# Kernel optimization log

Hardware: AMD Instinct MI355X
Metric: run time of the kernel (lower is better)

Reference implementation:

```python
import jax, jax.numpy as jnp
import numpy as np

D_MODEL = 1024
N_HEADS = 16
D_K = D_MODEL // N_HEADS
ROPE_THETA = 10000.0


def setup_inputs() -> dict:
    key = jax.random.key(0)
    ks = jax.random.split(key, 5)
    B, S = 2, 2048
    std = (2.0 / (D_MODEL + D_MODEL)) ** 0.5
    x = jax.random.normal(ks[0], (B, S, D_MODEL), dtype=jnp.float32)
    Wq = jax.random.normal(ks[1], (D_MODEL, D_MODEL), dtype=jnp.float32) * std
    Wk = jax.random.normal(ks[2], (D_MODEL, D_MODEL), dtype=jnp.float32) * std
    Wv = jax.random.normal(ks[3], (D_MODEL, D_MODEL), dtype=jnp.float32) * std
    Wo = jax.random.normal(ks[4], (D_MODEL, D_MODEL), dtype=jnp.float32) * std
    token_positions = jnp.arange(S, dtype=jnp.int64 if jax.config.jax_enable_x64 else jnp.int32)
    return {"x": x, "Wq": Wq, "Wk": Wk, "Wv": Wv, "Wo": Wo,
            "token_positions": token_positions}


def _apply_rope(t, token_positions):
    # t: [B, H, S, d_k]; token_positions: [S]
    inv_freq = 1.0 / (ROPE_THETA ** (jnp.arange(0, D_K, 2, dtype=jnp.float32) / D_K))  # [d_k/2]
    freqs = token_positions.astype(jnp.float32)[:, None] * inv_freq[None, :]  # [S, d_k/2]
    cos, sin = jnp.cos(freqs), jnp.sin(freqs)
    x1, x2 = t[..., ::2], t[..., 1::2]
    xr = x1 * cos - x2 * sin
    yr = x1 * sin + x2 * cos
    # interleave back to even/odd positions
    out = jnp.stack([xr, yr], axis=-1).reshape(t.shape)
    return out


def reference(x, Wq, Wk, Wv, Wo, token_positions):
    B, S, D = x.shape
    H, dk = N_HEADS, D_K
    # projections: weight is [d_out, d_in], applied as x @ W.T
    def proj_heads(W):
        y = jnp.einsum('bsd,ed->bse', x, W)
        return y.reshape(B, S, H, dk).transpose(0, 2, 1, 3)  # [B,H,S,dk]
    q = proj_heads(Wq)
    k = proj_heads(Wk)
    v = proj_heads(Wv)
    q = _apply_rope(q, token_positions)
    k = _apply_rope(k, token_positions)
    scores = jnp.einsum('bhqd,bhkd->bhqk', q, k) / jnp.sqrt(jnp.float32(dk))
    causal = jnp.tril(jnp.ones((S, S), dtype=bool))
    scores = jnp.where(causal, scores, -jnp.inf)
    attn = jax.nn.softmax(scores, axis=-1)
    out = jnp.einsum('bhqk,bhkd->bhqd', attn, v)  # [B,H,S,dk]
    out = out.transpose(0, 2, 1, 3).reshape(B, S, D)
    return jnp.einsum('bsd,ed->bse', out, Wo)
```

## Files before the change

kernel.cpp:

```cpp
#include <hip/hip_runtime.h>

typedef __bf16 bf16x8 __attribute__((ext_vector_type(8)));
typedef float f32x4 __attribute__((ext_vector_type(4)));
typedef unsigned short u16x8 __attribute__((ext_vector_type(8)));


__device__ __forceinline__ unsigned short f2bf(float f) {
  unsigned u = __builtin_bit_cast(unsigned, f);
  u = (u + 0x7FFFu + ((u >> 16) & 1u)) >> 16;
  return (unsigned short)u;
}

__device__ __forceinline__ void load_lds16(const void* g, void* l) {
  __builtin_amdgcn_global_load_lds(
      (__attribute__((address_space(1))) void*)g,
      (__attribute__((address_space(3))) void*)l, 16, 0, 0);
}

__global__ __launch_bounds__(256) void k_convert(
    const float* __restrict__ x,
    const float* __restrict__ wq, const float* __restrict__ wk,
    const float* __restrict__ wv, const float* __restrict__ wo,
    unsigned short* __restrict__ xb,
    unsigned short* __restrict__ wqb, unsigned short* __restrict__ wkb,
    unsigned short* __restrict__ wvb, unsigned short* __restrict__ wob) {
  const int g = blockIdx.x * 256 + threadIdx.x;
  const float* src;
  unsigned short* dst;
  int off;
  if (g < (1 << 20)) {
    src = x; dst = xb; off = g;
  } else {
    const int q = g - (1 << 20);
    const int t = q >> 18;
    off = q & ((1 << 18) - 1);
    src = (t == 0) ? wq : (t == 1) ? wk : (t == 2) ? wv : wo;
    dst = (t == 0) ? wqb : (t == 1) ? wkb : (t == 2) ? wvb : wob;
  }
  const float4 v = ((const float4*)src)[off];
  ushort4 r;
  r.x = f2bf(v.x); r.y = f2bf(v.y); r.z = f2bf(v.z); r.w = f2bf(v.w);
  ((ushort4*)dst)[off] = r;
}

__global__ __launch_bounds__(256) void k_rope_tab(const int* __restrict__ tpos,
                                                  float* __restrict__ ct,
                                                  float* __restrict__ st) {
  const int idx = blockIdx.x * 256 + threadIdx.x;
  const int s = idx >> 5, i = idx & 31;
  const double p = (double)tpos[s];
  const double f = p * pow(10000.0, -(double)(2 * i) / 64.0);
  ct[idx] = (float)cos(f);
  st[idx] = (float)sin(f);
}

__device__ __forceinline__ void gemm_core_1024(
    const unsigned short* __restrict__ Ag,
    const unsigned short* __restrict__ Bg,
    unsigned short* As, unsigned short* Bs, f32x4 (&acc)[4][4], int tid) {
  const int lane = tid & 63;
  const int w = tid >> 6;
  const int wm = (w >> 1) * 64;
  const int wn = (w & 1) * 64;
  const int lr = lane & 15;
  const int lg8 = (lane >> 4) * 8;
  const int c0 = tid, c1 = 256 + tid;
  const int ar0 = c0 >> 2, ac0 = (c0 & 3) * 8;
  const int ar1 = c1 >> 2, ac1 = (c1 & 3) * 8;

  auto stage = [&](int buf, int kt) {
    unsigned short* Ab = As + buf * 4096;
    unsigned short* Bb = Bs + buf * 4096;
    load_lds16(Ag + ar0 * 1024 + kt + ac0, Ab + c0 * 8);
    load_lds16(Ag + ar1 * 1024 + kt + ac1, Ab + c1 * 8);
    load_lds16(Bg + ar0 * 1024 + kt + ac0, Bb + c0 * 8);
    load_lds16(Bg + ar1 * 1024 + kt + ac1, Bb + c1 * 8);
  };

  stage(0, 0);
  stage(1, 32);
  int cur = 0;
  for (int ki = 0; ki < 32; ++ki) {
    if (ki + 2 < 32) {
      int nb = cur + 2; if (nb >= 3) nb -= 3;
      stage(nb, (ki + 2) * 32);
      asm volatile("s_waitcnt vmcnt(8)" ::: "memory");
    } else if (ki + 1 < 32) {
      asm volatile("s_waitcnt vmcnt(4)" ::: "memory");
    } else {
      asm volatile("s_waitcnt vmcnt(0)" ::: "memory");
    }
    __builtin_amdgcn_s_barrier();
    const unsigned short* Ab = As + cur * 4096;
    const unsigned short* Bb = Bs + cur * 4096;
    bf16x8 af[4], bfv[4];
#pragma unroll
    for (int mi = 0; mi < 4; ++mi)
      af[mi] = *(const bf16x8*)(Ab + (wm + mi * 16 + lr) * 32 + lg8);
#pragma unroll
    for (int ni = 0; ni < 4; ++ni)
      bfv[ni] = *(const bf16x8*)(Bb + (wn + ni * 16 + lr) * 32 + lg8);
    __builtin_amdgcn_s_setprio(1);
#pragma unroll
    for (int mi = 0; mi < 4; ++mi)
#pragma unroll
      for (int ni = 0; ni < 4; ++ni)
        acc[mi][ni] = __builtin_amdgcn_mfma_f32_16x16x32_bf16(
            af[mi], bfv[ni], acc[mi][ni], 0, 0, 0);
    __builtin_amdgcn_s_setprio(0);
    __builtin_amdgcn_s_barrier();
    ++cur; if (cur == 3) cur = 0;
  }
}

__global__ __launch_bounds__(256) void k_proj(
    const unsigned short* __restrict__ Xb,
    const unsigned short* __restrict__ Wq, const unsigned short* __restrict__ Wk,
    const unsigned short* __restrict__ Wv,
    const float* __restrict__ ctab, const float* __restrict__ stab,
    unsigned short* __restrict__ Qo, unsigned short* __restrict__ Ko,
    unsigned short* __restrict__ Vo) {
  __shared__ __align__(16) unsigned short As[3 * 128 * 32];
  __shared__ __align__(16) unsigned short Bs[3 * 128 * 32];
  const int z = blockIdx.z;
  const unsigned short* Wsel = (z == 0) ? Wq : (z == 1) ? Wk : Wv;
  unsigned short* Out = (z == 0) ? Qo : (z == 1) ? Ko : Vo;
  const int tid = threadIdx.x;
  const int bm = blockIdx.x * 128, bn = blockIdx.y * 128;
  f32x4 acc[4][4] = {};
  gemm_core_1024(Xb + (size_t)bm * 1024, Wsel + (size_t)bn * 1024, As, Bs, acc, tid);

  const int lane = tid & 63, w = tid >> 6;
  const int wm = (w >> 1) * 64, wn = (w & 1) * 64;
  const int lr = lane & 15, lg = lane >> 4;
  const bool rope = (z < 2);
  const bool odd = lane & 1;
#pragma unroll
  for (int mi = 0; mi < 4; ++mi) {
#pragma unroll
    for (int ni = 0; ni < 4; ++ni) {
#pragma unroll
      for (int reg = 0; reg < 4; ++reg) {
        const int r = bm + wm + mi * 16 + lg * 4 + reg;
        const int e = bn + wn + ni * 16 + lr;
        float val = acc[mi][ni][reg];
        const float partner = __shfl_xor(val, 1);
        const int s = r & 2047, b = r >> 11;
        const int h = e >> 6, d = e & 63;
        float outv = val;
        if (rope) {
          const int i = d >> 1;
          const float c = ctab[s * 32 + i];
          const float sn = stab[s * 32 + i];
          outv = odd ? (val * c + partner * sn) : (val * c - partner * sn);
        }
        if (z == 2)
          Out[((size_t)(b * 16 + h) * 64 + d) * 2048 + s] = f2bf(outv);
        else
          Out[((size_t)(b * 16 + h) * 2048 + s) * 64 + d] = f2bf(outv);
      }
    }
  }
}

__global__ __launch_bounds__(256, 2) void k_attn(
    const unsigned short* __restrict__ Q, const unsigned short* __restrict__ K,
    const unsigned short* __restrict__ Vt, unsigned short* __restrict__ O) {
  __shared__ __align__(16) unsigned short Vs[4][64 * 64];
  __shared__ __align__(16) unsigned short Pl[4][32 * 68];
  const int L = blockIdx.x + 16 * blockIdx.y;
  const int rr = L & 31;
  const int bh = (rr & 7) * 4 + (rr >> 3);
  const int a = L >> 5;
  const int qt = (a < 8) ? a : 23 - a;
  const int tid = threadIdx.x, lane = tid & 63, w = tid >> 6;
  const int lr = lane & 15, lg = lane >> 4;
  const unsigned short* Qg = Q + (size_t)bh * 2048 * 64;
  const unsigned short* Kg = K + (size_t)bh * 2048 * 64;
  const unsigned short* Vg = Vt + (size_t)bh * 64 * 2048;
  const int qrow = qt * 128 + w * 32;
  const int Tw = (qrow + 95) >> 6;
  unsigned short* Vw = &Vs[w][0];
  unsigned short* Pw = &Pl[w][0];

  bf16x8 qf[2][2];
#pragma unroll
  for (int mi = 0; mi < 2; ++mi)
#pragma unroll
    for (int h = 0; h < 2; ++h)
      qf[mi][h] = *(const bf16x8*)(Qg + (qrow + mi * 16 + lr) * 64 + h * 32 + lg * 8);

  u16x8 ouv;
#pragma unroll
  for (int j = 0; j < 8; ++j) ouv[j] = 0x3F80;
  const bf16x8 onesf = __builtin_bit_cast(bf16x8, ouv);

  f32x4 oacc[2][4] = {};
  float mrow[2][4], lrow[2][4];
#pragma unroll
  for (int mi = 0; mi < 2; ++mi)
#pragma unroll
    for (int r = 0; r < 4; ++r) { mrow[mi][r] = -__builtin_inff(); lrow[mi][r] = 0.f; }

  const float SCL = 0.125f * 1.44269504088896f;

  auto issueV = [&](int kv0) {
#pragma unroll
    for (int i = 0; i < 8; ++i) {
      const int r = i * 8 + (lane >> 3);
      const int j = lane & 7;
      load_lds16(Vg + (size_t)r * 2048 + kv0 + ((j ^ (r & 7)) * 8),
                 Vw + i * 512 + lane * 8);
    }
  };
  auto loadK = [&](bf16x8 (&kd)[4][2], int kv0) {
#pragma unroll
    for (int nt = 0; nt < 4; ++nt)
#pragma unroll
      for (int h = 0; h < 2; ++h)
        kd[nt][h] = *(const bf16x8*)(Kg + (size_t)(kv0 + nt * 16 + lr) * 64 +
                                     h * 32 + lg * 8);
  };

  bf16x8 kA[4][2], kB[4][2];
  loadK(kA, 0);
  issueV(0);

  auto body = [&](int t, bf16x8 (&kc)[4][2], bf16x8 (&kn)[4][2]) {
    const int kv0 = t * 64;
    const bool more = (t + 1 < Tw);
    if (more) loadK(kn, kv0 + 64);

    f32x4 sacc[2][4];
    __builtin_amdgcn_s_setprio(1);
#pragma unroll
    for (int nt = 0; nt < 4; ++nt) {
#pragma unroll
      for (int mi = 0; mi < 2; ++mi) {
        f32x4 z = {0.f, 0.f, 0.f, 0.f};
        z = __builtin_amdgcn_mfma_f32_16x16x32_bf16(qf[mi][0], kc[nt][0], z, 0, 0, 0);
        sacc[mi][nt] = __builtin_amdgcn_mfma_f32_16x16x32_bf16(qf[mi][1], kc[nt][1], z, 0, 0, 0);
      }
    }
    __builtin_amdgcn_s_setprio(0);

    const bool needmask = (t == Tw - 1);
    float pm[2][4];
#pragma unroll
    for (int mi = 0; mi < 2; ++mi)
#pragma unroll
      for (int r = 0; r < 4; ++r) pm[mi][r] = -__builtin_inff();
#pragma unroll
    for (int mi = 0; mi < 2; ++mi)
#pragma unroll
      for (int nt = 0; nt < 4; ++nt)
#pragma unroll
        for (int reg = 0; reg < 4; ++reg) {
          float sv = sacc[mi][nt][reg];
          if (needmask) {
            const int kg = kv0 + nt * 16 + lr;
            const int qg = qrow + mi * 16 + lg * 4 + reg;
            if (kg > qg) sv = -__builtin_inff();
          }
          sacc[mi][nt][reg] = sv;
          pm[mi][reg] = fmaxf(pm[mi][reg], sv);
        }
#pragma unroll
    for (int off = 1; off < 16; off <<= 1)
#pragma unroll
      for (int mi = 0; mi < 2; ++mi)
#pragma unroll
        for (int reg = 0; reg < 4; ++reg)
          pm[mi][reg] = fmaxf(pm[mi][reg], __shfl_xor(pm[mi][reg], off));

    float gm = -1.f;
#pragma unroll
    for (int mi = 0; mi < 2; ++mi)
#pragma unroll
      for (int reg = 0; reg < 4; ++reg)
        gm = fmaxf(gm, pm[mi][reg] - mrow[mi][reg]);
    float al[2][4], msc[2][4];
    if (__any(gm > 0.f)) {
#pragma unroll
      for (int mi = 0; mi < 2; ++mi)
#pragma unroll
        for (int reg = 0; reg < 4; ++reg) {
          const float mn = fmaxf(mrow[mi][reg], pm[mi][reg]);
          al[mi][reg] = exp2f(SCL * (mrow[mi][reg] - mn));
          mrow[mi][reg] = mn;
          msc[mi][reg] = SCL * mn;
#pragma unroll
          for (int nt = 0; nt < 4; ++nt) oacc[mi][nt][reg] *= al[mi][reg];
          lrow[mi][reg] *= al[mi][reg];
        }
    } else {
#pragma unroll
      for (int mi = 0; mi < 2; ++mi)
#pragma unroll
        for (int reg = 0; reg < 4; ++reg) msc[mi][reg] = SCL * mrow[mi][reg];
    }
#pragma unroll
    for (int mi = 0; mi < 2; ++mi)
#pragma unroll
      for (int nt = 0; nt < 4; ++nt)
#pragma unroll
        for (int reg = 0; reg < 4; ++reg)
          sacc[mi][nt][reg] = exp2f(sacc[mi][nt][reg] * SCL - msc[mi][reg]);

#pragma unroll
    for (int mi = 0; mi < 2; ++mi)
#pragma unroll
      for (int nt = 0; nt < 4; ++nt)
#pragma unroll
        for (int reg = 0; reg < 4; ++reg)
          Pw[(mi * 16 + lg * 4 + reg) * 68 + nt * 16 + lr] =
              f2bf(sacc[mi][nt][reg]);
    bf16x8 pa[2][2];
#pragma unroll
    for (int mi = 0; mi < 2; ++mi)
#pragma unroll
      for (int ks = 0; ks < 2; ++ks)
        pa[mi][ks] = *(const bf16x8*)(Pw + (mi * 16 + lr) * 68 + ks * 32 + lg * 8);

    if (more) asm volatile("s_waitcnt vmcnt(8)" ::: "memory");
    else      asm volatile("s_waitcnt vmcnt(0)" ::: "memory");

    __builtin_amdgcn_s_setprio(1);
#pragma unroll
    for (int mi = 0; mi < 2; ++mi) {
      f32x4 z = {0.f, 0.f, 0.f, 0.f};
      z = __builtin_amdgcn_mfma_f32_16x16x32_bf16(pa[mi][0], onesf, z, 0, 0, 0);
      z = __builtin_amdgcn_mfma_f32_16x16x32_bf16(pa[mi][1], onesf, z, 0, 0, 0);
#pragma unroll
      for (int reg = 0; reg < 4; ++reg) lrow[mi][reg] += z[reg];
    }
#pragma unroll
    for (int nt = 0; nt < 4; ++nt) {
      const int row = nt * 16 + lr;
      const bf16x8 vb0 = *(const bf16x8*)(Vw + row * 64 + ((lg ^ (row & 7)) * 8));
      const bf16x8 vb1 = *(const bf16x8*)(Vw + row * 64 + (((lg + 4) ^ (row & 7)) * 8));
#pragma unroll
      for (int mi = 0; mi < 2; ++mi) {
        oacc[mi][nt] = __builtin_amdgcn_mfma_f32_16x16x32_bf16(pa[mi][0], vb0,
                                                               oacc[mi][nt], 0, 0, 0);
        oacc[mi][nt] = __builtin_amdgcn_mfma_f32_16x16x32_bf16(pa[mi][1], vb1,
                                                               oacc[mi][nt], 0, 0, 0);
      }
    }
    __builtin_amdgcn_s_setprio(0);

    asm volatile("s_waitcnt lgkmcnt(0)" ::: "memory");
    if (more) issueV(kv0 + 64);
  };

  int t = 0;
  while (t < Tw) {
    body(t, kA, kB); ++t;
    if (t < Tw) { body(t, kB, kA); ++t; }
  }

  const int b = bh >> 4, h = bh & 15;
#pragma unroll
  for (int mi = 0; mi < 2; ++mi)
#pragma unroll
    for (int reg = 0; reg < 4; ++reg) {
      const float inv = 1.0f / lrow[mi][reg];
      const int s = qrow + mi * 16 + lg * 4 + reg;
#pragma unroll
      for (int nt = 0; nt < 4; ++nt) {
        const int dv = nt * 16 + lr;
        O[((size_t)b * 2048 + s) * 1024 + h * 64 + dv] = f2bf(oacc[mi][nt][reg] * inv);
      }
    }
}

__global__ __launch_bounds__(256) void k_out(const unsigned short* __restrict__ Ab,
                                             const unsigned short* __restrict__ Wo,
                                             float* __restrict__ Out) {
  __shared__ __align__(16) unsigned short As[3 * 128 * 32];
  __shared__ __align__(16) unsigned short Bs[3 * 128 * 32];
  const int tid = threadIdx.x;
  const int bm = blockIdx.x * 128, bn = blockIdx.y * 128;
  f32x4 acc[4][4] = {};
  gemm_core_1024(Ab + (size_t)bm * 1024, Wo + (size_t)bn * 1024, As, Bs, acc, tid);
  const int lane = tid & 63, w = tid >> 6;
  const int wm = (w >> 1) * 64, wn = (w & 1) * 64;
  const int lr = lane & 15, lg = lane >> 4;
#pragma unroll
  for (int mi = 0; mi < 4; ++mi)
#pragma unroll
    for (int ni = 0; ni < 4; ++ni)
#pragma unroll
      for (int reg = 0; reg < 4; ++reg) {
        const int r = bm + wm + mi * 16 + lg * 4 + reg;
        const int e = bn + wn + ni * 16 + lr;
        Out[(size_t)r * 1024 + e] = acc[mi][ni][reg];
      }
}

extern "C" void kernel_launch(void* const* d_in, const int* in_sizes, int n_in,
                              void* d_out, int out_size, void* d_ws, size_t ws_size,
                              hipStream_t stream) {
  const float* x = (const float*)d_in[0];
  const float* Wq = (const float*)d_in[1];
  const float* Wk = (const float*)d_in[2];
  const float* Wv = (const float*)d_in[3];
  const float* Wo = (const float*)d_in[4];
  const int* tpos = (const int*)d_in[5];
  float* out = (float*)d_out;
  char* ws = (char*)d_ws;
  const size_t MB = 1024 * 1024;
  unsigned short* xb = (unsigned short*)(ws);
  unsigned short* wqb = (unsigned short*)(ws + 8 * MB);
  unsigned short* wkb = (unsigned short*)(ws + 10 * MB);
  unsigned short* wvb = (unsigned short*)(ws + 12 * MB);
  unsigned short* wob = (unsigned short*)(ws + 14 * MB);
  unsigned short* Qb = (unsigned short*)(ws + 16 * MB);
  unsigned short* Kb = (unsigned short*)(ws + 24 * MB);
  unsigned short* Vtb = (unsigned short*)(ws + 32 * MB);
  unsigned short* Ab = (unsigned short*)(ws + 40 * MB);
  float* ctab = (float*)(ws + 48 * MB);
  float* stab = (float*)(ws + 48 * MB + 256 * 1024);

  k_convert<<<dim3(8192), dim3(256), 0, stream>>>(x, Wq, Wk, Wv, Wo, xb, wqb, wkb,
                                                  wvb, wob);
  k_rope_tab<<<dim3(256), dim3(256), 0, stream>>>(tpos, ctab, stab);
  k_proj<<<dim3(32, 8, 3), dim3(256), 0, stream>>>(xb, wqb, wkb, wvb, ctab, stab,
                                                   Qb, Kb, Vtb);
  k_attn<<<dim3(16, 32), dim3(256), 0, stream>>>(Qb, Kb, Vtb, Ab);
  k_out<<<dim3(32, 8), dim3(256), 0, stream>>>(Ab, wob, out);
}
```

Measured before the change: 185.0 us.

## Split attention into single-wave blocks pairing a short and long causal query tile

The attention kernel now launches 2048 single-wavefront blocks instead of 512 four-wave blocks. Each wave handles two 16-row query tiles, one near the start and one near the end of the sequence, so causal work per wave is balanced and every block does similar work. The two tiles share the same K register loads and V tiles staged in LDS. This trades per-block LDS sharing and 32-row MFMA reuse for finer load balance, at the cost of more blocks and more per-iteration branching.

```diff
diff --git a/kernel.cpp b/kernel.cpp
--- a/kernel.cpp
+++ b/kernel.cpp
@@ -163,215 +163,215 @@
   }
 }
 
-__global__ __launch_bounds__(256, 2) void k_attn(
+__global__ __launch_bounds__(64, 2) void k_attn(
     const unsigned short* __restrict__ Q, const unsigned short* __restrict__ K,
     const unsigned short* __restrict__ Vt, unsigned short* __restrict__ O) {
-  __shared__ __align__(16) unsigned short Vs[4][64 * 64];
-  __shared__ __align__(16) unsigned short Pl[4][32 * 68];
-  const int L = blockIdx.x + 16 * blockIdx.y;
-  const int rr = L & 31;
-  const int bh = (rr & 7) * 4 + (rr >> 3);
-  const int a = L >> 5;
-  const int qt = (a < 8) ? a : 23 - a;
-  const int tid = threadIdx.x, lane = tid & 63, w = tid >> 6;
+  __shared__ __align__(16) unsigned short Vs[64 * 64];
+  __shared__ __align__(16) unsigned short Pl[32 * 68];
+  const int L = blockIdx.x;
+  const int bh = (L & 7) * 4 + ((L >> 3) & 3);
+  const int p = L >> 5;
+  const int qrowA = p * 16, qrowB = (127 - p) * 16;
+  const int lane = threadIdx.x & 63;
   const int lr = lane & 15, lg = lane >> 4;
   const unsigned short* Qg = Q + (size_t)bh * 2048 * 64;
   const unsigned short* Kg = K + (size_t)bh * 2048 * 64;
   const unsigned short* Vg = Vt + (size_t)bh * 64 * 2048;
-  const int qrow = qt * 128 + w * 32;
-  const int Tw = (qrow + 95) >> 6;
-  unsigned short* Vw = &Vs[w][0];
-  unsigned short* Pw = &Pl[w][0];
-
-  bf16x8 qf[2][2];
-#pragma unroll
-  for (int mi = 0; mi < 2; ++mi)
-#pragma unroll
-    for (int h = 0; h < 2; ++h)
-      qf[mi][h] = *(const bf16x8*)(Qg + (qrow + mi * 16 + lr) * 64 + h * 32 + lg * 8);
+  const int Ta = (qrowA + 79) >> 6;
+  const int Tb = (qrowB + 79) >> 6;
+
+  bf16x8 qfA[2], qfB[2];
+#pragma unroll
+  for (int h = 0; h < 2; ++h) {
+    qfA[h] = *(const bf16x8*)(Qg + (qrowA + lr) * 64 + h * 32 + lg * 8);
+    qfB[h] = *(const bf16x8*)(Qg + (qrowB + lr) * 64 + h * 32 + lg * 8);
+  }
 
   u16x8 ouv;
 #pragma unroll
   for (int j = 0; j < 8; ++j) ouv[j] = 0x3F80;
   const bf16x8 onesf = __builtin_bit_cast(bf16x8, ouv);
 
-  f32x4 oacc[2][4] = {};
-  float mrow[2][4], lrow[2][4];
-#pragma unroll
-  for (int mi = 0; mi < 2; ++mi)
-#pragma unroll
-    for (int r = 0; r < 4; ++r) { mrow[mi][r] = -__builtin_inff(); lrow[mi][r] = 0.f; }
+  f32x4 oA[4] = {}, oB[4] = {};
+  float mA[4], lA[4], mB[4], lB[4];
+#pragma unroll
+  for (int r = 0; r < 4; ++r) {
+    mA[r] = -__builtin_inff(); lA[r] = 0.f;
+    mB[r] = -__builtin_inff(); lB[r] = 0.f;
+  }
 
   const float SCL = 0.125f * 1.44269504088896f;
 
-  auto issueV = [&](int kv0) {
-#pragma unroll
-    for (int i = 0; i < 8; ++i) {
-      const int r = i * 8 + (lane >> 3);
-      const int j = lane & 7;
-      load_lds16(Vg + (size_t)r * 2048 + kv0 + ((j ^ (r & 7)) * 8),
-                 Vw + i * 512 + lane * 8);
-    }
+  const int kbase = lr * 64 + lg * 8;
+  const unsigned short* Knext = Kg;
+  const int vbase = (lane >> 3) * 2048 + (((lane & 7) ^ (lane >> 3)) * 8);
+  const unsigned short* Vnext = Vg;
+  unsigned short* Vw = &Vs[0];
+
+  auto loadK = [&](bf16x8 (&kd)[4][2]) {
+#pragma unroll
+    for (int nt = 0; nt < 4; ++nt)
+#pragma unroll
+      for (int h = 0; h < 2; ++h)
+        kd[nt][h] = *(const bf16x8*)(Knext + nt * 1024 + h * 32 + kbase);
+    Knext += 4096;
   };
-  auto loadK = [&](bf16x8 (&kd)[4][2], int kv0) {
+  auto issueV = [&]() {
+#pragma unroll
+    for (int i0 = 0; i0 < 8; ++i0)
+      load_lds16(Vnext + i0 * 16384 + vbase, Vw + i0 * 512 + lane * 8);
+    Vnext += 64;
+  };
+
+  auto softmax = [&](f32x4 (&s)[4], float (&m)[4], float (&l)[4], f32x4 (&oa)[4],
+                     int qrow, bool needmask, int kv0, int rowbase) {
+    float pm[4];
+#pragma unroll
+    for (int r = 0; r < 4; ++r) pm[r] = -__builtin_inff();
 #pragma unroll
     for (int nt = 0; nt < 4; ++nt)
 #pragma unroll
-      for (int h = 0; h < 2; ++h)
-        kd[nt][h] = *(const bf16x8*)(Kg + (size_t)(kv0 + nt * 16 + lr) * 64 +
-                                     h * 32 + lg * 8);
+      for (int reg = 0; reg < 4; ++reg) {
+        float sv = s[nt][reg];
+        if (needmask) {
+          const int kg = kv0 + nt * 16 + lr;
+          const int qg = qrow + lg * 4 + reg;
+          if (kg > qg) sv = -__builtin_inff();
+        }
+        s[nt][reg] = sv;
+        pm[reg] = fmaxf(pm[reg], sv);
+      }
+#pragma unroll
+    for (int off = 1; off < 16; off <<= 1)
+#pragma unroll
+      for (int reg = 0; reg < 4; ++reg)
+        pm[reg] = fmaxf(pm[reg], __shfl_xor(pm[reg], off));
+
+    float gm = -1.f;
+#pragma unroll
+    for (int reg = 0; reg < 4; ++reg) gm = fmaxf(gm, pm[reg] - m[reg]);
+    float msc[4];
+    if (__any(gm > 0.f)) {
+#pragma unroll
+      for (int reg = 0; reg < 4; ++reg) {
+        const float mn = fmaxf(m[reg], pm[reg]);
+        const float al = exp2f(SCL * (m[reg] - mn));
+        m[reg] = mn;
+        msc[reg] = SCL * mn;
+        l[reg] *= al;
+#pragma unroll
+        for (int nt = 0; nt < 4; ++nt) oa[nt][reg] *= al;
+      }
+    } else {
+#pragma unroll
+      for (int reg = 0; reg < 4; ++reg) msc[reg] = SCL * m[reg];
+    }
+#pragma unroll
+    for (int nt = 0; nt < 4; ++nt)
+#pragma unroll
+      for (int reg = 0; reg < 4; ++reg) {
+        const float pv = exp2f(s[nt][reg] * SCL - msc[reg]);
+        Pl[(rowbase + lg * 4 + reg) * 68 + nt * 16 + lr] = f2bf(pv);
+      }
   };
 
-  bf16x8 kA[4][2], kB[4][2];
-  loadK(kA, 0);
-  issueV(0);
+  bf16x8 kA_[4][2], kB_[4][2];
+  loadK(kA_);
+  issueV();
 
   auto body = [&](int t, bf16x8 (&kc)[4][2], bf16x8 (&kn)[4][2]) {
     const int kv0 = t * 64;
-    const bool more = (t + 1 < Tw);
-    if (more) loadK(kn, kv0 + 64);
-
-    f32x4 sacc[2][4];
+    const bool more = (t + 1 < Tb);
+    const bool actA = (t < Ta);
+    if (more) loadK(kn);
+
+    f32x4 sB_[4];
     __builtin_amdgcn_s_setprio(1);
 #pragma unroll
     for (int nt = 0; nt < 4; ++nt) {
-#pragma unroll
-      for (int mi = 0; mi < 2; ++mi) {
+      f32x4 z = {0.f, 0.f, 0.f, 0.f};
+      z = __builtin_amdgcn_mfma_f32_16x16x32_bf16(qfB[0], kc[nt][0], z, 0, 0, 0);
+      sB_[nt] = __builtin_amdgcn_mfma_f32_16x16x32_bf16(qfB[1], kc[nt][1], z, 0, 0, 0);
+    }
+    __builtin_amdgcn_s_setprio(0);
+    softmax(sB_, mB, lB, oB, qrowB, t == Tb - 1, kv0, 16);
+
+    if (actA) {
+      f32x4 sA_[4];
+      __builtin_amdgcn_s_setprio(1);
+#pragma unroll
+      for (int nt = 0; nt < 4; ++nt) {
         f32x4 z = {0.f, 0.f, 0.f, 0.f};
-        z = __builtin_amdgcn_mfma_f32_16x16x32_bf16(qf[mi][0], kc[nt][0], z, 0, 0, 0);
-        sacc[mi][nt] = __builtin_amdgcn_mfma_f32_16x16x32_bf16(qf[mi][1], kc[nt][1], z, 0, 0, 0);
-      }
-    }
-    __builtin_amdgcn_s_setprio(0);
-
-    const bool needmask = (t == Tw - 1);
-    float pm[2][4];
-#pragma unroll
-    for (int mi = 0; mi < 2; ++mi)
-#pragma unroll
-      for (int r = 0; r < 4; ++r) pm[mi][r] = -__builtin_inff();
-#pragma unroll
-    for (int mi = 0; mi < 2; ++mi)
-#pragma unroll
-      for (int nt = 0; nt < 4; ++nt)
-#pragma unroll
-        for (int reg = 0; reg < 4; ++reg) {
-          float sv = sacc[mi][nt][reg];
-          if (needmask) {
-            const int kg = kv0 + nt * 16 + lr;
-            const int qg = qrow + mi * 16 + lg * 4 + reg;
-            if (kg > qg) sv = -__builtin_inff();
-          }
-          sacc[mi][nt][reg] = sv;
-          pm[mi][reg] = fmaxf(pm[mi][reg], sv);
-        }
-#pragma unroll
-    for (int off = 1; off < 16; off <<= 1)
-#pragma unroll
-      for (int mi = 0; mi < 2; ++mi)
-#pragma unroll
-        for (int reg = 0; reg < 4; ++reg)
-          pm[mi][reg] = fmaxf(pm[mi][reg], __shfl_xor(pm[mi][reg], off));
-
-    float gm = -1.f;
-#pragma unroll
-    for (int mi = 0; mi < 2; ++mi)
-#pragma unroll
-      for (int reg = 0; reg < 4; ++reg)
-        gm = fmaxf(gm, pm[mi][reg] - mrow[mi][reg]);
-    float al[2][4], msc[2][4];
-    if (__any(gm > 0.f)) {
-#pragma unroll
-      for (int mi = 0; mi < 2; ++mi)
-#pragma unroll
-        for (int reg = 0; reg < 4; ++reg) {
-          const float mn = fmaxf(mrow[mi][reg], pm[mi][reg]);
-          al[mi][reg] = exp2f(SCL * (mrow[mi][reg] - mn));
-          mrow[mi][reg] = mn;
-          msc[mi][reg] = SCL * mn;
-#pragma unroll
-          for (int nt = 0; nt < 4; ++nt) oacc[mi][nt][reg] *= al[mi][reg];
-          lrow[mi][reg] *= al[mi][reg];
-        }
-    } else {
-#pragma unroll
-      for (int mi = 0; mi < 2; ++mi)
-#pragma unroll
-        for (int reg = 0; reg < 4; ++reg) msc[mi][reg] = SCL * mrow[mi][reg];
-    }
-#pragma unroll
-    for (int mi = 0; mi < 2; ++mi)
-#pragma unroll
-      for (int nt = 0; nt < 4; ++nt)
-#pragma unroll
-        for (int reg = 0; reg < 4; ++reg)
-          sacc[mi][nt][reg] = exp2f(sacc[mi][nt][reg] * SCL - msc[mi][reg]);
-
-#pragma unroll
-    for (int mi = 0; mi < 2; ++mi)
-#pragma unroll
-      for (int nt = 0; nt < 4; ++nt)
-#pragma unroll
-        for (int reg = 0; reg < 4; ++reg)
-          Pw[(mi * 16 + lg * 4 + reg) * 68 + nt * 16 + lr] =
-              f2bf(sacc[mi][nt][reg]);
-    bf16x8 pa[2][2];
-#pragma unroll
-    for (int mi = 0; mi < 2; ++mi)
-#pragma unroll
-      for (int ks = 0; ks < 2; ++ks)
-        pa[mi][ks] = *(const bf16x8*)(Pw + (mi * 16 + lr) * 68 + ks * 32 + lg * 8);
+        z = __builtin_amdgcn_mfma_f32_16x16x32_bf16(qfA[0], kc[nt][0], z, 0, 0, 0);
+        sA_[nt] = __builtin_amdgcn_mfma_f32_16x16x32_bf16(qfA[1], kc[nt][1], z, 0, 0, 0);
+      }
+      __builtin_amdgcn_s_setprio(0);
+      softmax(sA_, mA, lA, oA, qrowA, t == Ta - 1, kv0, 0);
+    }
+
+    bf16x8 paA[2], paB[2];
+#pragma unroll
+    for (int ks = 0; ks < 2; ++ks) {
+      paB[ks] = *(const bf16x8*)(Pl + (16 + lr) * 68 + ks * 32 + lg * 8);
+      if (actA) paA[ks] = *(const bf16x8*)(Pl + lr * 68 + ks * 32 + lg * 8);
+    }
 
     if (more) asm volatile("s_waitcnt vmcnt(8)" ::: "memory");
     else      asm volatile("s_waitcnt vmcnt(0)" ::: "memory");
 
     __builtin_amdgcn_s_setprio(1);
-#pragma unroll
-    for (int mi = 0; mi < 2; ++mi) {
+    {
       f32x4 z = {0.f, 0.f, 0.f, 0.f};
-      z = __builtin_amdgcn_mfma_f32_16x16x32_bf16(pa[mi][0], onesf, z, 0, 0, 0);
-      z = __builtin_amdgcn_mfma_f32_16x16x32_bf16(pa[mi][1], onesf, z, 0, 0, 0);
-#pragma unroll
-      for (int reg = 0; reg < 4; ++reg) lrow[mi][reg] += z[reg];
+      z = __builtin_amdgcn_mfma_f32_16x16x32_bf16(paB[0], onesf, z, 0, 0, 0);
+      z = __builtin_amdgcn_mfma_f32_16x16x32_bf16(paB[1], onesf, z, 0, 0, 0);
+#pragma unroll
+      for (int reg = 0; reg < 4; ++reg) lB[reg] += z[reg];
+    }
+    if (actA) {
+      f32x4 z = {0.f, 0.f, 0.f, 0.f};
+      z = __builtin_amdgcn_mfma_f32_16x16x32_bf16(paA[0], onesf, z, 0, 0, 0);
+      z = __builtin_amdgcn_mfma_f32_16x16x32_bf16(paA[1], onesf, z, 0, 0, 0);
+#pragma unroll
+      for (int reg = 0; reg < 4; ++reg) lA[reg] += z[reg];
     }
 #pragma unroll
     for (int nt = 0; nt < 4; ++nt) {
       const int row = nt * 16 + lr;
       const bf16x8 vb0 = *(const bf16x8*)(Vw + row * 64 + ((lg ^ (row & 7)) * 8));
       const bf16x8 vb1 = *(const bf16x8*)(Vw + row * 64 + (((lg + 4) ^ (row & 7)) * 8));
-#pragma unroll
-      for (int mi = 0; mi < 2; ++mi) {
-        oacc[mi][nt] = __builtin_amdgcn_mfma_f32_16x16x32_bf16(pa[mi][0], vb0,
-                                                               oacc[mi][nt], 0, 0, 0);
-        oacc[mi][nt] = __builtin_amdgcn_mfma_f32_16x16x32_bf16(pa[mi][1], vb1,
-                                                               oacc[mi][nt], 0, 0, 0);
+      oB[nt] = __builtin_amdgcn_mfma_f32_16x16x32_bf16(paB[0], vb0, oB[nt], 0, 0, 0);
+      oB[nt] = __builtin_amdgcn_mfma_f32_16x16x32_bf16(paB[1], vb1, oB[nt], 0, 0, 0);
+      if (actA) {
+        oA[nt] = __builtin_amdgcn_mfma_f32_16x16x32_bf16(paA[0], vb0, oA[nt], 0, 0, 0);
+        oA[nt] = __builtin_amdgcn_mfma_f32_16x16x32_bf16(paA[1], vb1, oA[nt], 0, 0, 0);
       }
     }
     __builtin_amdgcn_s_setprio(0);
 
     asm volatile("s_waitcnt lgkmcnt(0)" ::: "memory");
-    if (more) issueV(kv0 + 64);
+    if (more) issueV();
   };
 
   int t = 0;
-  while (t < Tw) {
-    body(t, kA, kB); ++t;
-    if (t < Tw) { body(t, kB, kA); ++t; }
+  for (;;) {
+    body(t, kA_, kB_); ++t; if (t >= Tb) break;
+    body(t, kB_, kA_); ++t; if (t >= Tb) break;
   }
 
   const int b = bh >> 4, h = bh & 15;
 #pragma unroll
-  for (int mi = 0; mi < 2; ++mi)
-#pragma unroll
-    for (int reg = 0; reg < 4; ++reg) {
-      const float inv = 1.0f / lrow[mi][reg];
-      const int s = qrow + mi * 16 + lg * 4 + reg;
-#pragma unroll
-      for (int nt = 0; nt < 4; ++nt) {
-        const int dv = nt * 16 + lr;
-        O[((size_t)b * 2048 + s) * 1024 + h * 64 + dv] = f2bf(oacc[mi][nt][reg] * inv);
-      }
-    }
+  for (int reg = 0; reg < 4; ++reg) {
+    const float invA = 1.0f / lA[reg];
+    const float invB = 1.0f / lB[reg];
+    const int sA_ = qrowA + lg * 4 + reg;
+    const int sB_ = qrowB + lg * 4 + reg;
+#pragma unroll
+    for (int nt = 0; nt < 4; ++nt) {
+      const int dv = nt * 16 + lr;
+      O[((size_t)b * 2048 + sA_) * 1024 + h * 64 + dv] = f2bf(oA[nt][reg] * invA);
+      O[((size_t)b * 2048 + sB_) * 1024 + h * 64 + dv] = f2bf(oB[nt][reg] * invB);
+    }
+  }
 }
 
 __global__ __launch_bounds__(256) void k_out(const unsigned short* __restrict__ Ab,
@@ -427,6 +427,6 @@
   k_rope_tab<<<dim3(256), dim3(256), 0, stream>>>(tpos, ctab, stab);
   k_proj<<<dim3(32, 8, 3), dim3(256), 0, stream>>>(xb, wqb, wkb, wvb, ctab, stab,
                                                    Qb, Kb, Vtb);
-  k_attn<<<dim3(16, 32), dim3(256), 0, stream>>>(Qb, Kb, Vtb, Ab);
+  k_attn<<<dim3(2048), dim3(64), 0, stream>>>(Qb, Kb, Vtb, Ab);
   k_out<<<dim3(32, 8), dim3(256), 0, stream>>>(Ab, wob, out);
 }
```

After: 158.6 us. 1.17x faster.
